# Optimization experiments

Measured on AMD Instinct MI355X. Metric: run time of the kernel, lower is better.

## Reference

```python
import jax, jax.numpy as jnp
import numpy as np

B, C, L = 8, 256, 2048
RED = 8
CQK = C // RED  # 32


def setup_inputs() -> dict:
    key = jax.random.key(0)
    ks = jax.random.split(key, 8)
    s = 0.05
    x = jax.random.normal(ks[0], (B, C, L), dtype=jnp.float32)
    Wq = jax.random.normal(ks[1], (CQK, C), dtype=jnp.float32) * s
    bq = jax.random.normal(ks[2], (CQK,), dtype=jnp.float32) * s
    Wk = jax.random.normal(ks[3], (CQK, C), dtype=jnp.float32) * s
    bk = jax.random.normal(ks[4], (CQK,), dtype=jnp.float32) * s
    Wv = jax.random.normal(ks[5], (C, C), dtype=jnp.float32) * s
    bv = jax.random.normal(ks[6], (C,), dtype=jnp.float32) * s
    gamma = jnp.asarray([0.5], dtype=jnp.float32)  # learned scalar (init 0 in torch)
    return {"x": x, "Wq": Wq, "bq": bq, "Wk": Wk, "bk": bk, "Wv": Wv, "bv": bv, "gamma": gamma}


def reference(x, Wq, bq, Wk, bk, Wv, bv, gamma):
    # 1x1 Conv1d == channel-mixing matmul: [O,C] x [B,C,L] -> [B,O,L]
    q = jnp.einsum('oc,bcl->bol', Wq, x) + bq[:, None]   # [B,CQK,L]
    k = jnp.einsum('oc,bcl->bol', Wk, x) + bk[:, None]   # [B,CQK,L]
    v = jnp.einsum('oc,bcl->bol', Wv, x) + bv[:, None]   # [B,C,L]
    # attn[b,i,j] = softmax_j( q(:,i) . k(:,j) )  -- NOTE: no 1/sqrt(d) scaling
    scores = jnp.einsum('bci,bcj->bij', q, k)            # [B,L,L]
    attn = jax.nn.softmax(scores, axis=-1)
    # out[b,c,i] = sum_j v[b,c,j] * attn[b,i,j]
    out = jnp.einsum('bcj,bij->bci', v, attn)            # [B,C,L]
    return gamma[0] * out + x
```

## Files before the change

kernel.cpp:

```cpp
#include <hip/hip_runtime.h>

#define B 8
#define C 256
#define L 2048
#define CQK 32
#define SSEG 4
#define JSEG (L / SSEG)
#define NT (JSEG / 32)
#define SM_SHIFT2 28.8539008f

typedef unsigned short u16;
typedef __attribute__((ext_vector_type(8))) short bf8;
typedef __attribute__((ext_vector_type(4))) float f4;

__device__ __forceinline__ u16 f2bf(float f) {
    union { float f; unsigned u; } v; v.f = f;
    unsigned r = v.u + 0x7FFFu + ((v.u >> 16) & 1u);
    return (u16)(r >> 16);
}
__device__ __forceinline__ float bfl(unsigned u) {
    union { unsigned u; float f; } v; v.u = u << 16; return v.f;
}
__device__ __forceinline__ float bfh(unsigned u) {
    union { unsigned u; float f; } v; v.u = u & 0xFFFF0000u; return v.f;
}
__device__ __forceinline__ unsigned cvtpk(float lo, float hi) {
    unsigned r;
    asm("v_cvt_pk_bf16_f32 %0, %1, %2" : "=v"(r) : "v"(lo), "v"(hi));
    return r;
}
__device__ __forceinline__ float ex2(float x) {
    float r;
    asm("v_exp_f32 %0, %1" : "=v"(r) : "v"(x));
    return r;
}

__device__ __forceinline__ void gld16(const u16* gp, u16* lp) {
    auto* g1 = (const __attribute__((address_space(1))) u16*)gp;
    auto* l3 = (__attribute__((address_space(3))) u16*)lp;
    __builtin_amdgcn_global_load_lds(g1, l3, 16, 0, 0);
}
__device__ __forceinline__ void wait_vm0() {
    asm volatile("s_waitcnt vmcnt(0)" ::: "memory");
    __builtin_amdgcn_sched_barrier(0);
}
__device__ __forceinline__ void wait_vm2() {
    asm volatile("s_waitcnt vmcnt(2)" ::: "memory");
    __builtin_amdgcn_sched_barrier(0);
}
__device__ __forceinline__ void wait_lgkm0() {
    asm volatile("s_waitcnt lgkmcnt(0)" ::: "memory");
    __builtin_amdgcn_sched_barrier(0);
}
__device__ __forceinline__ void bar() {
    __builtin_amdgcn_sched_barrier(0);
    __builtin_amdgcn_s_barrier();
    __builtin_amdgcn_sched_barrier(0);
}

__global__ __launch_bounds__(256) void wconv(
    const float* __restrict__ Wq, const float* __restrict__ bq,
    const float* __restrict__ Wk, const float* __restrict__ bk,
    const float* __restrict__ Wv, const float* __restrict__ bv,
    u16* __restrict__ Wall, float* __restrict__ ball)
{
    const int idx = (blockIdx.x * 256 + threadIdx.x) * 4;
    const int row = idx >> 8, c = idx & 255;
    const float* s;
    if (row < 32)      s = Wq + row * C + c;
    else if (row < 64) s = Wk + (row - 32) * C + c;
    else               s = Wv + (row - 64) * C + c;
    const float4 v = *(const float4*)s;
    uint2 o;
    o.x = f2bf(v.x) | ((unsigned)f2bf(v.y) << 16);
    o.y = f2bf(v.z) | ((unsigned)f2bf(v.w) << 16);
    *(uint2*)(Wall + idx) = o;
    if (blockIdx.x == 0) {
        for (int i = threadIdx.x; i < 320; i += 256)
            ball[i] = (i < 32) ? bq[i] : (i < 64) ? bk[i - 32] : bv[i - 64];
    }
}

__global__ __launch_bounds__(256) void xconv(const float* __restrict__ x,
                                             u16* __restrict__ xt)
{
    __shared__ float tile[64][65];
    const int b = blockIdx.z, c0 = blockIdx.y * 64, l0 = blockIdx.x * 64;
    const int t = threadIdx.x;
    const int ln = t & 63, w = t >> 6;
#pragma unroll
    for (int i = 0; i < 16; i++) {
        const int c = w * 16 + i;
        tile[c][ln] = x[((size_t)(b * C + c0 + c)) * L + l0 + ln];
    }
    __syncthreads();
    const int lrow = t >> 2, q = t & 3;
    unsigned o[8];
#pragma unroll
    for (int jj = 0; jj < 8; jj++) {
        const float a0 = tile[q * 16 + jj * 2][lrow];
        const float a1 = tile[q * 16 + jj * 2 + 1][lrow];
        o[jj] = f2bf(a0) | ((unsigned)f2bf(a1) << 16);
    }
    u16* dst = xt + ((size_t)(b * L + l0 + lrow)) * 256 + c0 + q * 16;
    *(uint4*)(dst)     = make_uint4(o[0], o[1], o[2], o[3]);
    *(uint4*)(dst + 8) = make_uint4(o[4], o[5], o[6], o[7]);
}

__global__ __launch_bounds__(256) void proj(
    const u16* __restrict__ xt, const u16* __restrict__ Wall,
    const float* __restrict__ ball, u16* __restrict__ qt,
    u16* __restrict__ kt, u16* __restrict__ vv)
{
    __shared__ u16 xlds[32 * 256];
    const int b = blockIdx.y, l0 = blockIdx.x * 32;
    const int t = threadIdx.x, w = t >> 6, ln = t & 63;
    const int lc = ln & 15, g = ln >> 4;

#pragma unroll
    for (int mm = 0; mm < 4; mm++) {
        const int cg = t + mm * 256;
        const int lrow = cg >> 5, phys = cg & 31;
        const int logical = (phys & 24) | ((phys & 7) ^ (lrow & 7));
        gld16(xt + ((size_t)(b * L + l0 + lrow)) * 256 + logical * 8,
              xlds + (size_t)(w * 64 + mm * 256) * 8);
    }
    __syncthreads();

    f4 acc[5][2];
#pragma unroll
    for (int rt = 0; rt < 5; rt++) {
        const int row0 = (w * 5 + rt) * 16 + g * 4;
        const float4 bi = *(const float4*)(ball + row0);
#pragma unroll
        for (int ct = 0; ct < 2; ct++) {
            acc[rt][ct].x = bi.x; acc[rt][ct].y = bi.y;
            acc[rt][ct].z = bi.z; acc[rt][ct].w = bi.w;
        }
    }

#pragma unroll
    for (int k = 0; k < 8; k++) {
        bf8 bfr[2];
#pragma unroll
        for (int ct = 0; ct < 2; ct++) {
            const int lrow = ct * 16 + lc;
            const int lchunk = k * 4 + g;
            const int phys = (lchunk & 24) | ((lchunk & 7) ^ (lrow & 7));
            bfr[ct] = *(const bf8*)(xlds + (size_t)lrow * 256 + phys * 8);
        }
#pragma unroll
        for (int rt = 0; rt < 5; rt++) {
            const bf8 af = *(const bf8*)(Wall +
                (size_t)((w * 5 + rt) * 16 + lc) * 256 + k * 32 + g * 8);
#pragma unroll
            for (int ct = 0; ct < 2; ct++)
                acc[rt][ct] = __builtin_amdgcn_mfma_f32_16x16x32_bf16(
                    af, bfr[ct], acc[rt][ct], 0, 0, 0);
        }
    }

    const float Q_SCALE = 1.44269504f;
#pragma unroll
    for (int rt = 0; rt < 5; rt++) {
        const int rg = w * 5 + rt;
        const int row0 = rg * 16 + g * 4;
#pragma unroll
        for (int ct = 0; ct < 2; ct++) {
            const int l = l0 + ct * 16 + lc;
            const f4 a = acc[rt][ct];
            if (rg < 2) {
                uint2 o;
                o.x = f2bf(a.x * Q_SCALE) | ((unsigned)f2bf(a.y * Q_SCALE) << 16);
                o.y = f2bf(a.z * Q_SCALE) | ((unsigned)f2bf(a.w * Q_SCALE) << 16);
                *(uint2*)(qt + ((size_t)(b * L + l)) * 32 + row0) = o;
            } else if (rg < 4) {
                uint2 o;
                o.x = f2bf(a.x) | ((unsigned)f2bf(a.y) << 16);
                o.y = f2bf(a.z) | ((unsigned)f2bf(a.w) << 16);
                *(uint2*)(kt + ((size_t)(b * L + l)) * 32 + (row0 - 32)) = o;
            } else {
                const int c = row0 - 64;
                vv[((size_t)(b * C + c + 0)) * L + l] = f2bf(a.x);
                vv[((size_t)(b * C + c + 1)) * L + l] = f2bf(a.y);
                vv[((size_t)(b * C + c + 2)) * L + l] = f2bf(a.z);
                vv[((size_t)(b * C + c + 3)) * L + l] = f2bf(a.w);
            }
        }
    }
}

__global__ __launch_bounds__(512, 4) void attn(
    const u16* __restrict__ qt, const u16* __restrict__ kt,
    const u16* __restrict__ vv, u16* __restrict__ po,
    float* __restrict__ plsum)
{
    __shared__ u16 vsw[8][2][1024];
    __shared__ u16 ps[2][64][40];
    __shared__ float fl[64];

    const int fid = blockIdx.x;
    const int win = fid & 31, bx = fid >> 5;
    const int b = win >> 2, sidx = win & 3;
    const int t = threadIdx.x, w = t >> 6, ln = t & 63;
    const int lc = ln & 15, g = ln >> 4;
    const int i0 = bx * 64;
    const int js = sidx * JSEG;
    const int wc0 = w * 32;
    const int tb = (b * 32 + bx) * SSEG + sidx;

    const int r0 = ln >> 2, s0 = ln & 3;
    const int gch = s0 ^ (r0 & 3) ^ ((r0 >> 2) & 3);
    const u16* vsrc = vv + ((size_t)(b * C + wc0 + r0)) * L + js + gch * 8;

    f4 acc[4][2];
    const f4 fz = {0.f, 0.f, 0.f, 0.f};
#pragma unroll
    for (int it = 0; it < 4; it++)
#pragma unroll
        for (int ct = 0; ct < 2; ct++) acc[it][ct] = fz;
    float lsum = 0.f;

    bf8 qf = {}, kf0 = {}, kf1 = {};
    const u16* kb = kt;
    if (w < 4) {
        qf = *(const bf8*)(qt + ((size_t)(b * L + i0 + w * 16 + lc)) * 32 + g * 8);
        kb = kt + ((size_t)(b * L + js + lc)) * 32 + g * 8;
    }

    auto stage = [&](int buf, int jt) {
        const u16* s = vsrc + jt * 32;
        u16* d = &vsw[w][buf][0];
        gld16(s, d);
        gld16(s + (size_t)16 * L, d + 512);
    };
    auto kload = [&](int jt) {
        asm volatile("global_load_dwordx4 %0, %1, off"
                     : "=&v"(kf0) : "v"(kb + (size_t)(jt * 32) * 32) : "memory");
        asm volatile("global_load_dwordx4 %0, %1, off"
                     : "=&v"(kf1) : "v"(kb + (size_t)(jt * 32 + 16) * 32) : "memory");
    };

    stage(0, 0);
    if (w < 4) kload(0);
    int cur = 0;

    const int sread = (g ^ (lc & 3) ^ ((lc >> 2) & 3)) * 8;

#pragma unroll 1
    for (int jt = 0; jt < NT; jt++) {
        if (jt + 1 < NT) {
            stage(cur ^ 1, jt + 1);
            wait_vm2();
        } else {
            wait_vm0();
        }

        if (w < 4) {
            const f4 sA = __builtin_amdgcn_mfma_f32_16x16x32_bf16(kf0, qf, fz, 0, 0, 0);
            const f4 sB = __builtin_amdgcn_mfma_f32_16x16x32_bf16(kf1, qf, fz, 0, 0, 0);
            if (jt + 1 < NT) kload(jt + 1);
            const float p0 = ex2(sA.x - SM_SHIFT2);
            const float p1 = ex2(sA.y - SM_SHIFT2);
            const float p2 = ex2(sA.z - SM_SHIFT2);
            const float p3 = ex2(sA.w - SM_SHIFT2);
            const float p4 = ex2(sB.x - SM_SHIFT2);
            const float p5 = ex2(sB.y - SM_SHIFT2);
            const float p6 = ex2(sB.z - SM_SHIFT2);
            const float p7 = ex2(sB.w - SM_SHIFT2);
            uint2 oa, ob;
            oa.x = cvtpk(p0, p1); oa.y = cvtpk(p2, p3);
            ob.x = cvtpk(p4, p5); ob.y = cvtpk(p6, p7);
            *(uint2*)(&ps[jt & 1][w * 16 + lc][g * 4]) = oa;
            *(uint2*)(&ps[jt & 1][w * 16 + lc][16 + g * 4]) = ob;
            float psum = ((p0 + p1) + (p2 + p3)) + ((p4 + p5) + (p6 + p7));
            psum += __shfl_xor(psum, 16);
            psum += __shfl_xor(psum, 32);
            lsum += psum;
        }

        wait_lgkm0();
        bar();

        const u16* rb = &vsw[w][cur][0];
        __builtin_amdgcn_s_setprio(1);
#pragma unroll
        for (int ct = 0; ct < 2; ct++) {
            const bf8 vfr = *(const bf8*)(rb + ct * 512 + lc * 32 + sread);
#pragma unroll
            for (int it = 0; it < 4; it++) {
                const bf8 paf = *(const bf8*)(&ps[jt & 1][it * 16 + lc][0] + g * 8);
                acc[it][ct] = __builtin_amdgcn_mfma_f32_16x16x32_bf16(
                    paf, vfr, acc[it][ct], 0, 0, 0);
            }
        }
        __builtin_amdgcn_s_setprio(0);
        cur ^= 1;
    }

    if (w < 4) {
        fl[w * 16 + lc] = 1.0f / lsum;
        if (g == 0) plsum[(size_t)tb * 64 + w * 16 + lc] = lsum;
    }
    __syncthreads();
    u16* pob = po + (size_t)tb * 16384 + (size_t)(w & 1) * 2048
                  + ((size_t)(w >> 1) * 64 + g * 16 + lc) * 8;
#pragma unroll
    for (int it = 0; it < 4; it++) {
        const float4 iv = *(const float4*)&fl[it * 16 + g * 4];
        const f4 a0 = acc[it][0];
        const f4 a1 = acc[it][1];
        uint4 o;
        o.x = cvtpk(a0.x * iv.x, a0.y * iv.y);
        o.y = cvtpk(a0.z * iv.z, a0.w * iv.w);
        o.z = cvtpk(a1.x * iv.x, a1.y * iv.y);
        o.w = cvtpk(a1.z * iv.z, a1.w * iv.w);
        *(uint4*)(pob + (size_t)it * 4096) = o;
    }
}

__global__ __launch_bounds__(256) void combine(
    const u16* __restrict__ po, const float* __restrict__ plsum,
    const float* __restrict__ x, const float* __restrict__ gamma_p,
    float* __restrict__ out)
{
    __shared__ float raw[4][16];
    __shared__ float wts[4][16];
    const int bx = blockIdx.x, b = blockIdx.y, z = blockIdx.z;
    const int t = threadIdx.x, wq = t >> 6, ln = t & 63;
    const int lc = ln & 15, g = ln >> 4;
    const int tbase = (b * 32 + bx) * SSEG;

    if (t < 64)
        raw[t >> 4][t & 15] = plsum[(size_t)(tbase + (t >> 4)) * 64 + z * 16 + (t & 15)];
    __syncthreads();
    if (t < 16) {
        const float l0 = raw[0][t], l1 = raw[1][t], l2 = raw[2][t], l3 = raw[3][t];
        const float inv = 1.0f / (((l0 + l1) + (l2 + l3)));
        wts[0][t] = l0 * inv; wts[1][t] = l1 * inv;
        wts[2][t] = l2 * inv; wts[3][t] = l3 * inv;
    }
    __syncthreads();

    f4 tot[4];
    const f4 fz = {0.f, 0.f, 0.f, 0.f};
#pragma unroll
    for (int ct = 0; ct < 4; ct++) tot[ct] = fz;

#pragma unroll
    for (int s = 0; s < SSEG; s++) {
        const u16* base = po + ((size_t)(tbase + s) * 2048 + (size_t)z * 2 * 256 + t) * 8;
        const uint4 q0 = *(const uint4*)base;
        const uint4 q1 = *(const uint4*)(base + 2048);
        const float4 wv = *(const float4*)&wts[s][g * 4];
        tot[0].x += wv.x * bfl(q0.x); tot[0].y += wv.y * bfh(q0.x);
        tot[0].z += wv.z * bfl(q0.y); tot[0].w += wv.w * bfh(q0.y);
        tot[1].x += wv.x * bfl(q0.z); tot[1].y += wv.y * bfh(q0.z);
        tot[1].z += wv.z * bfl(q0.w); tot[1].w += wv.w * bfh(q0.w);
        tot[2].x += wv.x * bfl(q1.x); tot[2].y += wv.y * bfh(q1.x);
        tot[2].z += wv.z * bfl(q1.y); tot[2].w += wv.w * bfh(q1.y);
        tot[3].x += wv.x * bfl(q1.z); tot[3].y += wv.y * bfh(q1.z);
        tot[3].z += wv.z * bfl(q1.w); tot[3].w += wv.w * bfh(q1.w);
    }

    const float gmm = gamma_p[0];
#pragma unroll
    for (int ct = 0; ct < 4; ct++) {
        const int c = wq * 64 + ct * 16 + lc;
        const size_t adr = ((size_t)(b * C + c)) * L + bx * 64 + z * 16 + g * 4;
        const float4 xv = *(const float4*)(x + adr);
        float4 o;
        o.x = gmm * tot[ct].x + xv.x;
        o.y = gmm * tot[ct].y + xv.y;
        o.z = gmm * tot[ct].z + xv.z;
        o.w = gmm * tot[ct].w + xv.w;
        *(float4*)(out + adr) = o;
    }
}

extern "C" void kernel_launch(void* const* d_in, const int* in_sizes, int n_in,
                              void* d_out, int out_size, void* d_ws, size_t ws_size,
                              hipStream_t stream) {
    const float* x  = (const float*)d_in[0];
    const float* Wq = (const float*)d_in[1];
    const float* bq = (const float*)d_in[2];
    const float* Wk = (const float*)d_in[3];
    const float* bk = (const float*)d_in[4];
    const float* Wv = (const float*)d_in[5];
    const float* bv = (const float*)d_in[6];
    const float* gm = (const float*)d_in[7];
    float* out = (float*)d_out;

    u16* vvp  = (u16*)d_ws;
    u16* qtp  = vvp + (size_t)B * C * L;
    u16* ktp  = qtp + (size_t)B * L * CQK;
    u16* Wall = ktp + (size_t)B * L * CQK;
    float* ball = (float*)(Wall + 320 * 256);
    u16* xt   = Wall + 320 * 256 + 640;
    u16* po   = xt;
    float* plsum = (float*)(po + (size_t)B * 32 * SSEG * 2048 * 8);

    wconv<<<80, 256, 0, stream>>>(Wq, bq, Wk, bk, Wv, bv, Wall, ball);
    xconv<<<dim3(L / 64, C / 64, B), 256, 0, stream>>>(x, xt);
    proj<<<dim3(L / 32, B), 256, 0, stream>>>(xt, Wall, ball, qtp, ktp, vvp);
    attn<<<1024, 512, 0, stream>>>(qtp, ktp, vvp, po, plsum);
    combine<<<dim3(L / 64, B, SSEG), 256, 0, stream>>>(po, plsum, x, gm, out);
}
```

Measured before the change: 73.64 us.

## Drop split-K attention segments and fuse combine epilogue into attention kernel

Removes the four-way split of the key dimension, so each block walks the full sequence with 1024 threads (16 waves, 16 channels each) and writes the final gamma-scaled residual output directly. This eliminates the partial-output buffer, the partial-sum buffer and the separate combine kernel launch. In exchange the grid shrinks from 1024 to 256 blocks, and each block runs a serial loop four times longer. This may underfill the GPU's compute units and lengthen per-block latency.

```diff
diff --git a/kernel.cpp b/kernel.cpp
--- a/kernel.cpp
+++ b/kernel.cpp
@@ -4,9 +4,7 @@
 #define C 256
 #define L 2048
 #define CQK 32
-#define SSEG 4
-#define JSEG (L / SSEG)
-#define NT (JSEG / 32)
+#define NT (L / 32)
 #define SM_SHIFT2 28.8539008f
 
 typedef unsigned short u16;
@@ -18,12 +16,6 @@
     unsigned r = v.u + 0x7FFFu + ((v.u >> 16) & 1u);
     return (u16)(r >> 16);
 }
-__device__ __forceinline__ float bfl(unsigned u) {
-    union { unsigned u; float f; } v; v.u = u << 16; return v.f;
-}
-__device__ __forceinline__ float bfh(unsigned u) {
-    union { unsigned u; float f; } v; v.u = u & 0xFFFF0000u; return v.f;
-}
 __device__ __forceinline__ unsigned cvtpk(float lo, float hi) {
     unsigned r;
     asm("v_cvt_pk_bf16_f32 %0, %1, %2" : "=v"(r) : "v"(lo), "v"(hi));
@@ -44,8 +36,8 @@
     asm volatile("s_waitcnt vmcnt(0)" ::: "memory");
     __builtin_amdgcn_sched_barrier(0);
 }
-__device__ __forceinline__ void wait_vm2() {
-    asm volatile("s_waitcnt vmcnt(2)" ::: "memory");
+__device__ __forceinline__ void wait_vm1() {
+    asm volatile("s_waitcnt vmcnt(1)" ::: "memory");
     __builtin_amdgcn_sched_barrier(0);
 }
 __device__ __forceinline__ void wait_lgkm0() {
@@ -190,49 +182,41 @@
     }
 }
 
-__global__ __launch_bounds__(512, 4) void attn(
+__global__ __launch_bounds__(1024, 4) void attn(
     const u16* __restrict__ qt, const u16* __restrict__ kt,
-    const u16* __restrict__ vv, u16* __restrict__ po,
-    float* __restrict__ plsum)
+    const u16* __restrict__ vv, const float* __restrict__ x,
+    const float* __restrict__ gamma_p, float* __restrict__ out)
 {
-    __shared__ u16 vsw[8][2][1024];
+    __shared__ u16 vsw[16][2][512];
     __shared__ u16 ps[2][64][40];
     __shared__ float fl[64];
 
     const int fid = blockIdx.x;
-    const int win = fid & 31, bx = fid >> 5;
-    const int b = win >> 2, sidx = win & 3;
+    const int b = fid & 7, bx = fid >> 3;
     const int t = threadIdx.x, w = t >> 6, ln = t & 63;
     const int lc = ln & 15, g = ln >> 4;
     const int i0 = bx * 64;
-    const int js = sidx * JSEG;
-    const int wc0 = w * 32;
-    const int tb = (b * 32 + bx) * SSEG + sidx;
+    const int wc0 = w * 16;
 
     const int r0 = ln >> 2, s0 = ln & 3;
     const int gch = s0 ^ (r0 & 3) ^ ((r0 >> 2) & 3);
-    const u16* vsrc = vv + ((size_t)(b * C + wc0 + r0)) * L + js + gch * 8;
-
-    f4 acc[4][2];
+    const u16* vsrc = vv + ((size_t)(b * C + wc0 + r0)) * L + gch * 8;
+
+    f4 acc[4];
     const f4 fz = {0.f, 0.f, 0.f, 0.f};
 #pragma unroll
-    for (int it = 0; it < 4; it++)
-#pragma unroll
-        for (int ct = 0; ct < 2; ct++) acc[it][ct] = fz;
+    for (int it = 0; it < 4; it++) acc[it] = fz;
     float lsum = 0.f;
 
     bf8 qf = {}, kf0 = {}, kf1 = {};
     const u16* kb = kt;
     if (w < 4) {
         qf = *(const bf8*)(qt + ((size_t)(b * L + i0 + w * 16 + lc)) * 32 + g * 8);
-        kb = kt + ((size_t)(b * L + js + lc)) * 32 + g * 8;
+        kb = kt + ((size_t)(b * L + lc)) * 32 + g * 8;
     }
 
     auto stage = [&](int buf, int jt) {
-        const u16* s = vsrc + jt * 32;
-        u16* d = &vsw[w][buf][0];
-        gld16(s, d);
-        gld16(s + (size_t)16 * L, d + 512);
+        gld16(vsrc + jt * 32, &vsw[w][buf][0]);
     };
     auto kload = [&](int jt) {
         asm volatile("global_load_dwordx4 %0, %1, off"
@@ -251,7 +235,7 @@
     for (int jt = 0; jt < NT; jt++) {
         if (jt + 1 < NT) {
             stage(cur ^ 1, jt + 1);
-            wait_vm2();
+            wait_vm1();
         } else {
             wait_vm0();
         }
@@ -284,96 +268,33 @@
 
         const u16* rb = &vsw[w][cur][0];
         __builtin_amdgcn_s_setprio(1);
-#pragma unroll
-        for (int ct = 0; ct < 2; ct++) {
-            const bf8 vfr = *(const bf8*)(rb + ct * 512 + lc * 32 + sread);
+        {
+            const bf8 vfr = *(const bf8*)(rb + lc * 32 + sread);
 #pragma unroll
             for (int it = 0; it < 4; it++) {
                 const bf8 paf = *(const bf8*)(&ps[jt & 1][it * 16 + lc][0] + g * 8);
-                acc[it][ct] = __builtin_amdgcn_mfma_f32_16x16x32_bf16(
-                    paf, vfr, acc[it][ct], 0, 0, 0);
+                acc[it] = __builtin_amdgcn_mfma_f32_16x16x32_bf16(
+                    paf, vfr, acc[it], 0, 0, 0);
             }
         }
         __builtin_amdgcn_s_setprio(0);
         cur ^= 1;
     }
 
-    if (w < 4) {
-        fl[w * 16 + lc] = 1.0f / lsum;
-        if (g == 0) plsum[(size_t)tb * 64 + w * 16 + lc] = lsum;
-    }
+    if (w < 4) fl[w * 16 + lc] = 1.0f / lsum;
     __syncthreads();
-    u16* pob = po + (size_t)tb * 16384 + (size_t)(w & 1) * 2048
-                  + ((size_t)(w >> 1) * 64 + g * 16 + lc) * 8;
+    const float gmm = gamma_p[0];
+    const int c = wc0 + lc;
 #pragma unroll
     for (int it = 0; it < 4; it++) {
         const float4 iv = *(const float4*)&fl[it * 16 + g * 4];
-        const f4 a0 = acc[it][0];
-        const f4 a1 = acc[it][1];
-        uint4 o;
-        o.x = cvtpk(a0.x * iv.x, a0.y * iv.y);
-        o.y = cvtpk(a0.z * iv.z, a0.w * iv.w);
-        o.z = cvtpk(a1.x * iv.x, a1.y * iv.y);
-        o.w = cvtpk(a1.z * iv.z, a1.w * iv.w);
-        *(uint4*)(pob + (size_t)it * 4096) = o;
-    }
-}
-
-__global__ __launch_bounds__(256) void combine(
-    const u16* __restrict__ po, const float* __restrict__ plsum,
-    const float* __restrict__ x, const float* __restrict__ gamma_p,
-    float* __restrict__ out)
-{
-    __shared__ float raw[4][16];
-    __shared__ float wts[4][16];
-    const int bx = blockIdx.x, b = blockIdx.y, z = blockIdx.z;
-    const int t = threadIdx.x, wq = t >> 6, ln = t & 63;
-    const int lc = ln & 15, g = ln >> 4;
-    const int tbase = (b * 32 + bx) * SSEG;
-
-    if (t < 64)
-        raw[t >> 4][t & 15] = plsum[(size_t)(tbase + (t >> 4)) * 64 + z * 16 + (t & 15)];
-    __syncthreads();
-    if (t < 16) {
-        const float l0 = raw[0][t], l1 = raw[1][t], l2 = raw[2][t], l3 = raw[3][t];
-        const float inv = 1.0f / (((l0 + l1) + (l2 + l3)));
-        wts[0][t] = l0 * inv; wts[1][t] = l1 * inv;
-        wts[2][t] = l2 * inv; wts[3][t] = l3 * inv;
-    }
-    __syncthreads();
-
-    f4 tot[4];
-    const f4 fz = {0.f, 0.f, 0.f, 0.f};
-#pragma unroll
-    for (int ct = 0; ct < 4; ct++) tot[ct] = fz;
-
-#pragma unroll
-    for (int s = 0; s < SSEG; s++) {
-        const u16* base = po + ((size_t)(tbase + s) * 2048 + (size_t)z * 2 * 256 + t) * 8;
-        const uint4 q0 = *(const uint4*)base;
-        const uint4 q1 = *(const uint4*)(base + 2048);
-        const float4 wv = *(const float4*)&wts[s][g * 4];
-        tot[0].x += wv.x * bfl(q0.x); tot[0].y += wv.y * bfh(q0.x);
-        tot[0].z += wv.z * bfl(q0.y); tot[0].w += wv.w * bfh(q0.y);
-        tot[1].x += wv.x * bfl(q0.z); tot[1].y += wv.y * bfh(q0.z);
-        tot[1].z += wv.z * bfl(q0.w); tot[1].w += wv.w * bfh(q0.w);
-        tot[2].x += wv.x * bfl(q1.x); tot[2].y += wv.y * bfh(q1.x);
-        tot[2].z += wv.z * bfl(q1.y); tot[2].w += wv.w * bfh(q1.y);
-        tot[3].x += wv.x * bfl(q1.z); tot[3].y += wv.y * bfh(q1.z);
-        tot[3].z += wv.z * bfl(q1.w); tot[3].w += wv.w * bfh(q1.w);
-    }
-
-    const float gmm = gamma_p[0];
-#pragma unroll
-    for (int ct = 0; ct < 4; ct++) {
-        const int c = wq * 64 + ct * 16 + lc;
-        const size_t adr = ((size_t)(b * C + c)) * L + bx * 64 + z * 16 + g * 4;
+        const size_t adr = ((size_t)(b * C + c)) * L + i0 + it * 16 + g * 4;
         const float4 xv = *(const float4*)(x + adr);
         float4 o;
-        o.x = gmm * tot[ct].x + xv.x;
-        o.y = gmm * tot[ct].y + xv.y;
-        o.z = gmm * tot[ct].z + xv.z;
-        o.w = gmm * tot[ct].w + xv.w;
+        o.x = gmm * acc[it].x * iv.x + xv.x;
+        o.y = gmm * acc[it].y * iv.y + xv.y;
+        o.z = gmm * acc[it].z * iv.z + xv.z;
+        o.w = gmm * acc[it].w * iv.w + xv.w;
         *(float4*)(out + adr) = o;
     }
 }
@@ -397,12 +318,9 @@
     u16* Wall = ktp + (size_t)B * L * CQK;
     float* ball = (float*)(Wall + 320 * 256);
     u16* xt   = Wall + 320 * 256 + 640;
-    u16* po   = xt;
-    float* plsum = (float*)(po + (size_t)B * 32 * SSEG * 2048 * 8);
 
     wconv<<<80, 256, 0, stream>>>(Wq, bq, Wk, bk, Wv, bv, Wall, ball);
     xconv<<<dim3(L / 64, C / 64, B), 256, 0, stream>>>(x, xt);
     proj<<<dim3(L / 32, B), 256, 0, stream>>>(xt, Wall, ball, qtp, ktp, vvp);
-    attn<<<1024, 512, 0, stream>>>(qtp, ktp, vvp, po, plsum);
-    combine<<<dim3(L / 64, B, SSEG), 256, 0, stream>>>(po, plsum, x, gm, out);
-}
+    attn<<<256, 1024, 0, stream>>>(qtp, ktp, vvp, x, gm, out);
+}
```

Result: slower. 88.14 us (+19.7%).
